# Optimization experiments

Measured on AMD Instinct MI355X. Metric: run time of the kernel, lower is better.

The kernel has to match this reference:

```python
import jax, jax.numpy as jnp
import numpy as np

NEG = -1e9  # stand-in for -inf mask fill (avoids NaN, softmax weight ~0)
EPS = 1e-5  # torch LayerNorm default


def layer_norm(x, g, b):
    mu = jnp.mean(x, axis=-1, keepdims=True)
    var = jnp.mean(jnp.square(x - mu), axis=-1, keepdims=True)
    return (x - mu) * jax.lax.rsqrt(var + EPS) * g + b


def _forward(x, context, batch_lengths, max_len,
             Wq1, Wk1, Wv1, Wq2, Wk2, Wv2,
             ln1_g, ln1_b, ln2_g, ln2_b, ln3_g, ln3_b,
             fc1_w, fc1_b, fc2_w, fc2_b):
    B, L, E = x.shape
    H, _, dk = Wq1.shape
    pos = jnp.arange(L)
    valid = pos[None, :] < batch_lengths[:, None]                  # [B,L]
    out_mask = valid[:, :, None].astype(x.dtype)                   # [B,L,1] (outputMask)
    key_bias = jnp.where(valid, 0.0, NEG)[:, None, None, :]        # [B,1,1,L] (attnMask on keys)
    causal_bias = jnp.where(pos[:, None] >= pos[None, :], 0.0, NEG)  # [L,L] decoding mask
    scale = 1.0 / jnp.sqrt(jnp.asarray(dk, x.dtype))

    def mha(qk_src, v_src, Wq, Wk, Wv, causal):
        # Q,K from qk_src, V from v_src (faithful to Head.forward)
        m = out_mask[:, None]                                      # [B,1,L,1]
        Q = jnp.einsum('ble,hed->bhld', qk_src, Wq) * m
        K = jnp.einsum('ble,hed->bhld', qk_src, Wk) * m
        V = jnp.einsum('ble,hed->bhld', v_src, Wv) * m
        e = jnp.einsum('bhid,bhjd->bhij', Q, K) + key_bias
        if causal:
            e = e + causal_bias
        s = jax.nn.softmax(e * scale, axis=-1)
        o = jnp.einsum('bhij,bhjd->bhid', s, V)
        return o.transpose(0, 2, 1, 3).reshape(B, L, E)            # concat heads

    z = mha(x, x, Wq1, Wk1, Wv1, causal=True) * out_mask
    x1 = layer_norm(x + z, ln1_g, ln1_b)
    # cross block: Q,K from context, V from x1 (as in source)
    z = mha(context, x1, Wq2, Wk2, Wv2, causal=False) * out_mask
    x2 = layer_norm(x1 + z, ln2_g, ln2_b)
    h = jax.nn.relu(x2 @ fc1_w + fc1_b) * out_mask
    z = (h @ fc2_w + fc2_b) * out_mask
    return layer_norm(x2 + z, ln3_g, ln3_b)


def setup_inputs() -> dict:
    B, L, E, H = 8, 1024, 1024, 16
    dk = E // H
    key = jax.random.key(0)
    ks = jax.random.split(key, 16)
    w = lambda k, s: jax.random.normal(k, s, jnp.float32) * 0.02
    return {
        'x': jax.random.normal(ks[0], (B, L, E), jnp.float32),
        'context': jax.random.normal(ks[1], (B, L, E), jnp.float32),
        'batch_lengths': jax.random.randint(ks[2], (B,), 1, L + 1),
        'max_len': L,
        'Wq1': w(ks[3], (H, E, dk)), 'Wk1': w(ks[4], (H, E, dk)), 'Wv1': w(ks[5], (H, E, dk)),
        'Wq2': w(ks[6], (H, E, dk)), 'Wk2': w(ks[7], (H, E, dk)), 'Wv2': w(ks[8], (H, E, dk)),
        'ln1_g': jnp.ones((E,), jnp.float32), 'ln1_b': jnp.zeros((E,), jnp.float32),
        'ln2_g': jnp.ones((E,), jnp.float32), 'ln2_b': jnp.zeros((E,), jnp.float32),
        'ln3_g': jnp.ones((E,), jnp.float32), 'ln3_b': jnp.zeros((E,), jnp.float32),
        'fc1_w': w(ks[9], (E, E)), 'fc1_b': jnp.zeros((E,), jnp.float32),
        'fc2_w': w(ks[10], (E, E)), 'fc2_b': jnp.zeros((E,), jnp.float32),
    }


def reference(x, context, batch_lengths, max_len,
              Wq1, Wk1, Wv1, Wq2, Wk2, Wv2,
              ln1_g, ln1_b, ln2_g, ln2_b, ln3_g, ln3_b,
              fc1_w, fc1_b, fc2_w, fc2_b):
    return _forward(x, context, batch_lengths, max_len,
                    Wq1, Wk1, Wv1, Wq2, Wk2, Wv2,
                    ln1_g, ln1_b, ln2_g, ln2_b, ln3_g, ln3_b,
                    fc1_w, fc1_b, fc2_w, fc2_b)
```

## Files before the change

### kernel.cpp

```cpp
#include <hip/hip_runtime.h>


typedef unsigned short u16;
typedef unsigned int u32;
typedef __attribute__((ext_vector_type(8))) short bf16x8;
typedef __attribute__((ext_vector_type(4))) float f32x4;

#define Bv 8
#define Lv 1024
#define Ev 1024
#define Hv 16
#define DKv 64
#define Mv (Bv * Lv)

#if defined(__has_builtin)
# if __has_builtin(__builtin_amdgcn_global_load_lds)
#  define HAS_GLL 1
# endif
#endif
#ifndef HAS_GLL
# define HAS_GLL 0
#endif

#if HAS_GLL
__device__ __forceinline__ void gll16(const u16* g, u16* l) {
    __builtin_amdgcn_global_load_lds(
        (const __attribute__((address_space(1))) void*)(unsigned long long)(g),
        (__attribute__((address_space(3))) void*)(unsigned)(unsigned long long)(l),
        16, 0, 0);
}
#endif

__device__ __forceinline__ u16 f2bf(float f) {
    u32 u = __float_as_uint(f);
    u += 0x7fffu + ((u >> 16) & 1u);
    return (u16)(u >> 16);
}
__device__ __forceinline__ u32 pack2(float a, float b) {
    u32 ua = __float_as_uint(a); ua += 0x7fffu + ((ua >> 16) & 1u);
    u32 ub = __float_as_uint(b); ub += 0x7fffu + ((ub >> 16) & 1u);
    return (ua >> 16) | (ub & 0xffff0000u);
}
__device__ __forceinline__ float bf_lo(u32 u) { return __uint_as_float(u << 16); }
__device__ __forceinline__ float bf_hi(u32 u) { return __uint_as_float(u & 0xffff0000u); }

__global__ __launch_bounds__(256) void conv_k(const float* __restrict__ s, u16* __restrict__ d) {
    int i4 = (blockIdx.x * 256 + threadIdx.x) * 4;
    float4 v = *(const float4*)(s + i4);
    uint2 o = {pack2(v.x, v.y), pack2(v.z, v.w)};
    *(uint2*)(d + i4) = o;
}

__global__ __launch_bounds__(256) void trans_attn(const float* __restrict__ s, u16* __restrict__ d) {
    __shared__ float t[32][33];
    const int d0 = blockIdx.x * 32, e0 = blockIdx.y * 32, h = blockIdx.z;
    const int tx = threadIdx.x, ty = threadIdx.y;
#pragma unroll
    for (int i = 0; i < 4; i++)
        t[ty + i * 8][tx] = s[(size_t)h * Ev * DKv + (size_t)(e0 + ty + i * 8) * DKv + d0 + tx];
    __syncthreads();
#pragma unroll
    for (int i = 0; i < 4; i++)
        d[(size_t)(h * DKv + d0 + ty + i * 8) * Ev + e0 + tx] = f2bf(t[tx][ty + i * 8]);
}

__global__ __launch_bounds__(256) void trans_fc(const float* __restrict__ s, u16* __restrict__ d) {
    __shared__ float t[32][33];
    const int n0 = blockIdx.x * 32, k0 = blockIdx.y * 32;
    const int tx = threadIdx.x, ty = threadIdx.y;
#pragma unroll
    for (int i = 0; i < 4; i++)
        t[ty + i * 8][tx] = s[(size_t)(k0 + ty + i * 8) * Ev + n0 + tx];
    __syncthreads();
#pragma unroll
    for (int i = 0; i < 4; i++)
        d[(size_t)(n0 + ty + i * 8) * Ev + k0 + tx] = f2bf(t[tx][ty + i * 8]);
}

template <int BIAS, int RELU, int TRANSW>
__global__ __launch_bounds__(256) void mgemm(const u16* __restrict__ A,
                                             const u16* __restrict__ Wt,
                                             const float* __restrict__ bias,
                                             u16* __restrict__ O0, u16* __restrict__ O1,
                                             u16* __restrict__ O2,
                                             const int* __restrict__ lens) {
    __shared__ u16 Alds[16 * 512];
    __shared__ u16 Blds[16 * 512];
    const int tid = threadIdx.x;
    const int w = tid >> 6, l = tid & 63;
    const int lc = l & 15, lq = l >> 4;
    const int row0 = blockIdx.y * 128, col0 = blockIdx.x * 128;
    const int which = col0 >> 10, colL = col0 & 1023;
    u16* C = (which == 0) ? O0 : (which == 1 ? O1 : O2);
    const int wm4 = (w >> 1) * 4, wn4 = (w & 1) * 4;

    f32x4 acc[4][4];
#pragma unroll
    for (int i = 0; i < 4; i++)
#pragma unroll
        for (int j = 0; j < 4; j++) acc[i][j] = (f32x4){0.f, 0.f, 0.f, 0.f};

    const u16* Ag[4]; const u16* Bg[4]; u16* Al[4]; u16* Bl[4];
#pragma unroll
    for (int i = 0; i < 4; i++) {
        const int g16 = 2 * w + (i >> 1), k32 = i & 1;
        Ag[i] = A  + (size_t)(row0 + g16 * 16 + lc) * Ev + k32 * 32 + lq * 8;
        Bg[i] = Wt + (size_t)(col0 + g16 * 16 + lc) * Ev + k32 * 32 + lq * 8;
        Al[i] = Alds + (g16 * 2 + k32) * 512;
        Bl[i] = Blds + (g16 * 2 + k32) * 512;
    }

    for (int k0 = 0; k0 < Ev; k0 += 64) {
#if HAS_GLL
#pragma unroll
        for (int i = 0; i < 4; i++) { gll16(Ag[i], Al[i]); gll16(Bg[i], Bl[i]); }
#else
#pragma unroll
        for (int i = 0; i < 4; i++) {
            *(uint4*)(Al[i] + l * 8) = *(const uint4*)Ag[i];
            *(uint4*)(Bl[i] + l * 8) = *(const uint4*)Bg[i];
        }
#endif
#pragma unroll
        for (int i = 0; i < 4; i++) { Ag[i] += 64; Bg[i] += 64; }
        __syncthreads();
#pragma unroll
        for (int km = 0; km < 2; km++) {
            bf16x8 af[4], bfr[4];
#pragma unroll
            for (int mt = 0; mt < 4; mt++)
                af[mt] = *(const bf16x8*)(Alds + ((wm4 + mt) * 2 + km) * 512 + l * 8);
#pragma unroll
            for (int nt = 0; nt < 4; nt++)
                bfr[nt] = *(const bf16x8*)(Blds + ((wn4 + nt) * 2 + km) * 512 + l * 8);
#pragma unroll
            for (int mt = 0; mt < 4; mt++)
#pragma unroll
                for (int nt = 0; nt < 4; nt++)
                    acc[mt][nt] = __builtin_amdgcn_mfma_f32_16x16x32_bf16(
                        af[mt], bfr[nt], acc[mt][nt], 0, 0, 0);
        }
        __syncthreads();
    }

    int len = lens[row0 >> 10];
    len = min(max(len, 0), Lv);
    const bool tr = (TRANSW == which);
    float bv[4];
#pragma unroll
    for (int nt = 0; nt < 4; nt++)
        bv[nt] = BIAS ? bias[colL + wn4 * 16 + nt * 16 + lc] : 0.f;

#pragma unroll
    for (int mt = 0; mt < 4; mt++) {
        const int rowb = row0 + wm4 * 16 + mt * 16 + lq * 4;
#pragma unroll
        for (int nt = 0; nt < 4; nt++) {
            const int col = colL + wn4 * 16 + nt * 16 + lc;
            float v[4];
#pragma unroll
            for (int r = 0; r < 4; r++) {
                float x = acc[mt][nt][r] + bv[nt];
                if (RELU) x = fmaxf(x, 0.f);
                v[r] = (((rowb + r) & (Lv - 1)) >= len) ? 0.f : x;
            }
            if (tr) {
                uint2 o = {pack2(v[0], v[1]), pack2(v[2], v[3])};
                *(uint2*)(C + (size_t)col * Mv + rowb) = o;
            } else {
#pragma unroll
                for (int r = 0; r < 4; r++)
                    C[(size_t)(rowb + r) * Ev + col] = f2bf(v[r]);
            }
        }
    }
}

template <int CAUSAL>
__global__ __launch_bounds__(256) void mattn(u16* __restrict__ QZ,
                                             const u16* __restrict__ K,
                                             const u16* __restrict__ VT,
                                             const int* __restrict__ lens) {
    __shared__ u16 Kt[16 * 512];
    __shared__ u16 Vt[16 * 512];
    __shared__ u16 Pt[4 * 4 * 512];
    const int b = blockIdx.z, h = blockIdx.y, qb = blockIdx.x;
    const int q0 = qb * 128;
    const int tid = threadIdx.x;
    const int w = tid >> 6, l = tid & 63;
    const int lc = l & 15, lq = l >> 4;
    int len = lens[b];
    len = min(max(len, 0), Lv);

    if (q0 >= len) {
        const int zr = tid >> 1, zc = (tid & 1) * 32;
        uint4 z4 = {0u, 0u, 0u, 0u};
        uint4* p = (uint4*)(QZ + (size_t)(b * Lv + q0 + zr) * Ev + h * DKv + zc);
        p[0] = z4; p[1] = z4; p[2] = z4; p[3] = z4;
        return;
    }

    bf16x8 qf[2][2];
#pragma unroll
    for (int mt = 0; mt < 2; mt++)
#pragma unroll
        for (int k2 = 0; k2 < 2; k2++)
            qf[mt][k2] = *(const bf16x8*)(QZ + (size_t)(b * Lv + q0 + w * 32 + mt * 16 + lc) * Ev +
                                          h * DKv + k2 * 32 + lq * 8);

    f32x4 of[2][4];
#pragma unroll
    for (int mt = 0; mt < 2; mt++)
#pragma unroll
        for (int nd = 0; nd < 4; nd++) of[mt][nd] = (f32x4){0.f, 0.f, 0.f, 0.f};
    float mrow[2][4], lrow[2][4];
#pragma unroll
    for (int mt = 0; mt < 2; mt++)
#pragma unroll
        for (int r = 0; r < 4; r++) { mrow[mt][r] = -1e30f; lrow[mt][r] = 0.f; }

    const u16* Kg[4]; const u16* Vg[4]; u16* Kl[4]; u16* Vl[4];
#pragma unroll
    for (int i = 0; i < 4; i++) {
        const int k16 = 2 * w + (i >> 1), d32 = i & 1;
        Kg[i] = K + (size_t)(b * Lv + k16 * 16 + lc) * Ev + h * DKv + d32 * 32 + lq * 8;
        Kl[i] = Kt + (k16 * 2 + d32) * 512;
        Vg[i] = VT + (size_t)(h * DKv + w * 16 + lc) * Mv + b * Lv + i * 32 + lq * 8;
        Vl[i] = Vt + (w * 4 + i) * 512;
    }
    u16* Pw = Pt + w * 2048;

    const int jend = CAUSAL ? min(len, q0 + 128) : len;
    const int ntiles = (jend + 127) >> 7;

    for (int kt = 0; kt < ntiles; kt++) {
        const int koff = kt * 128;
#if HAS_GLL
#pragma unroll
        for (int i = 0; i < 4; i++) {
            gll16(Kg[i] + (size_t)koff * Ev, Kl[i]);
            gll16(Vg[i] + koff, Vl[i]);
        }
#else
#pragma unroll
        for (int i = 0; i < 4; i++) {
            *(uint4*)(Kl[i] + l * 8) = *(const uint4*)(Kg[i] + (size_t)koff * Ev);
            *(uint4*)(Vl[i] + l * 8) = *(const uint4*)(Vg[i] + koff);
        }
#endif
        __syncthreads();

        f32x4 sf[2][8];
#pragma unroll
        for (int nt = 0; nt < 8; nt++) {
            bf16x8 kf0 = *(const bf16x8*)(Kt + (nt * 2 + 0) * 512 + l * 8);
            bf16x8 kf1 = *(const bf16x8*)(Kt + (nt * 2 + 1) * 512 + l * 8);
#pragma unroll
            for (int mt = 0; mt < 2; mt++) {
                f32x4 s = (f32x4){0.f, 0.f, 0.f, 0.f};
                s = __builtin_amdgcn_mfma_f32_16x16x32_bf16(qf[mt][0], kf0, s, 0, 0, 0);
                s = __builtin_amdgcn_mfma_f32_16x16x32_bf16(qf[mt][1], kf1, s, 0, 0, 0);
                sf[mt][nt] = s;
            }
        }

        float alpha[2][4];
#pragma unroll
        for (int mt = 0; mt < 2; mt++) {
            float tmax[4] = {-1e30f, -1e30f, -1e30f, -1e30f};
#pragma unroll
            for (int nt = 0; nt < 8; nt++) {
                const int jj = koff + nt * 16 + lc;
                const bool jv = jj < len;
#pragma unroll
                for (int r = 0; r < 4; r++) {
                    const int iq = q0 + w * 32 + mt * 16 + lq * 4 + r;
                    const bool valid = jv && (!CAUSAL || jj <= iq);
                    float e = valid ? sf[mt][nt][r] * 0.125f : -1e30f;
                    sf[mt][nt][r] = e;
                    tmax[r] = fmaxf(tmax[r], e);
                }
            }
#pragma unroll
            for (int r = 0; r < 4; r++) {
#pragma unroll
                for (int d = 1; d < 16; d <<= 1)
                    tmax[r] = fmaxf(tmax[r], __shfl_xor(tmax[r], d, 64));
            }
            float psum[4];
#pragma unroll
            for (int r = 0; r < 4; r++) {
                const float mn = fmaxf(mrow[mt][r], tmax[r]);
                alpha[mt][r] = __expf(mrow[mt][r] - mn);
                mrow[mt][r] = mn;
                psum[r] = 0.f;
            }
#pragma unroll
            for (int nt = 0; nt < 8; nt++)
#pragma unroll
                for (int r = 0; r < 4; r++) {
                    float p = __expf(sf[mt][nt][r] - mrow[mt][r]);
                    sf[mt][nt][r] = p;
                    psum[r] += p;
                }
#pragma unroll
            for (int r = 0; r < 4; r++) {
#pragma unroll
                for (int d = 1; d < 16; d <<= 1) psum[r] += __shfl_xor(psum[r], d, 64);
                lrow[mt][r] = lrow[mt][r] * alpha[mt][r] + psum[r];
            }
#pragma unroll
            for (int nd = 0; nd < 4; nd++)
#pragma unroll
                for (int r = 0; r < 4; r++) of[mt][nd][r] *= alpha[mt][r];
        }

#pragma unroll
        for (int mt = 0; mt < 2; mt++) {
#pragma unroll
            for (int nt = 0; nt < 8; nt++)
#pragma unroll
                for (int r = 0; r < 4; r++)
                    Pw[(nt >> 1) * 512 +
                       ((2 * (nt & 1) + (lc >> 3)) * 16 + lq * 4 + r) * 8 + (lc & 7)] =
                        f2bf(sf[mt][nt][r]);
#pragma unroll
            for (int km = 0; km < 4; km++) {
                bf16x8 pa = *(const bf16x8*)(Pw + km * 512 + l * 8);
#pragma unroll
                for (int nd = 0; nd < 4; nd++) {
                    bf16x8 vb = *(const bf16x8*)(Vt + (nd * 4 + km) * 512 + l * 8);
                    of[mt][nd] = __builtin_amdgcn_mfma_f32_16x16x32_bf16(pa, vb, of[mt][nd], 0, 0, 0);
                }
            }
        }
        __syncthreads();
    }

#pragma unroll
    for (int mt = 0; mt < 2; mt++) {
        float inv[4];
#pragma unroll
        for (int r = 0; r < 4; r++) {
            const int iq = q0 + w * 32 + mt * 16 + lq * 4 + r;
            inv[r] = (iq < len && lrow[mt][r] > 0.f) ? (1.f / lrow[mt][r]) : 0.f;
        }
#pragma unroll
        for (int nd = 0; nd < 4; nd++)
#pragma unroll
            for (int r = 0; r < 4; r++)
                QZ[(size_t)(b * Lv + q0 + w * 32 + mt * 16 + lq * 4 + r) * Ev +
                   h * DKv + nd * 16 + lc] = f2bf(of[mt][nd][r] * inv[r]);
    }
}

template <int BASEBF, int OUTF32>
__global__ __launch_bounds__(256) void ln_k(const void* __restrict__ base,
                                            const u16* __restrict__ z,
                                            const float* __restrict__ g,
                                            const float* __restrict__ bta,
                                            void* __restrict__ out) {
    __shared__ float r1[256], r2[256];
    const int row = blockIdx.x, t = threadIdx.x;
    const int c0 = t * 4;
    float v[4];
    if (BASEBF) {
        uint2 bu = *(const uint2*)((const u16*)base + (size_t)row * Ev + c0);
        v[0] = bf_lo(bu.x); v[1] = bf_hi(bu.x); v[2] = bf_lo(bu.y); v[3] = bf_hi(bu.y);
    } else {
        float4 f = *(const float4*)((const float*)base + (size_t)row * Ev + c0);
        v[0] = f.x; v[1] = f.y; v[2] = f.z; v[3] = f.w;
    }
    uint2 zu = *(const uint2*)(z + (size_t)row * Ev + c0);
    v[0] += bf_lo(zu.x); v[1] += bf_hi(zu.x); v[2] += bf_lo(zu.y); v[3] += bf_hi(zu.y);
    r1[t] = v[0] + v[1] + v[2] + v[3];
    r2[t] = v[0] * v[0] + v[1] * v[1] + v[2] * v[2] + v[3] * v[3];
    __syncthreads();
    for (int s = 128; s > 0; s >>= 1) {
        if (t < s) { r1[t] += r1[t + s]; r2[t] += r2[t + s]; }
        __syncthreads();
    }
    const float mu = r1[0] * (1.f / Ev);
    const float var = r2[0] * (1.f / Ev) - mu * mu;
    const float rinv = rsqrtf(fmaxf(var, 0.f) + 1e-5f);
    float4 gv = *(const float4*)(g + c0);
    float4 bv = *(const float4*)(bta + c0);
    float y[4];
    y[0] = (v[0] - mu) * rinv * gv.x + bv.x;
    y[1] = (v[1] - mu) * rinv * gv.y + bv.y;
    y[2] = (v[2] - mu) * rinv * gv.z + bv.z;
    y[3] = (v[3] - mu) * rinv * gv.w + bv.w;
    if (OUTF32) {
        float4 ow = {y[0], y[1], y[2], y[3]};
        *(float4*)((float*)out + (size_t)row * Ev + c0) = ow;
    } else {
        uint2 ow = {pack2(y[0], y[1]), pack2(y[2], y[3])};
        *(uint2*)((u16*)out + (size_t)row * Ev + c0) = ow;
    }
}

extern "C" void kernel_launch(void* const* d_in, const int* in_sizes, int n_in,
                              void* d_out, int out_size, void* d_ws, size_t ws_size,
                              hipStream_t stream) {
    const float* x    = (const float*)d_in[0];
    const float* ctx  = (const float*)d_in[1];
    const int*   lens = (const int*)d_in[2];
    const float* Wq1 = (const float*)d_in[4];
    const float* Wk1 = (const float*)d_in[5];
    const float* Wv1 = (const float*)d_in[6];
    const float* Wq2 = (const float*)d_in[7];
    const float* Wk2 = (const float*)d_in[8];
    const float* Wv2 = (const float*)d_in[9];
    const float* g1 = (const float*)d_in[10], *b1 = (const float*)d_in[11];
    const float* g2 = (const float*)d_in[12], *b2 = (const float*)d_in[13];
    const float* g3 = (const float*)d_in[14], *b3 = (const float*)d_in[15];
    const float* fc1w = (const float*)d_in[16], *fc1b = (const float*)d_in[17];
    const float* fc2w = (const float*)d_in[18], *fc2b = (const float*)d_in[19];

    const size_t WSZ = (size_t)Ev * Ev;
    const size_t MM  = (size_t)Mv * Ev;
    u16* WT = (u16*)d_ws;
    u16* Wtq1 = WT + 0 * WSZ, *Wtk1 = WT + 1 * WSZ, *Wtv1 = WT + 2 * WSZ;
    u16* Wtq2 = WT + 3 * WSZ, *Wtk2 = WT + 4 * WSZ, *Wtv2 = WT + 5 * WSZ;
    u16* Wtf1 = WT + 6 * WSZ, *Wtf2 = WT + 7 * WSZ;
    u16* B1 = WT + 8 * WSZ;
    u16* B2 = B1 + MM;
    u16* B3 = B2 + MM;
    u16* B4 = B3 + MM;
    u16* xb = (u16*)d_out;
    u16* cb = xb + MM;

    dim3 gC(Mv * Ev / 1024), gTA(2, 32, Hv), gTF(32, 32), bT(32, 8);
    dim3 gQKV(24, 64), gQK(16, 64), gG1(8, 64), gA(8, Hv, Bv), gL(Mv);

    conv_k<<<gC, 256, 0, stream>>>(x, xb);
    conv_k<<<gC, 256, 0, stream>>>(ctx, cb);
    trans_attn<<<gTA, bT, 0, stream>>>(Wq1, Wtq1);
    trans_attn<<<gTA, bT, 0, stream>>>(Wk1, Wtk1);
    trans_attn<<<gTA, bT, 0, stream>>>(Wv1, Wtv1);
    trans_attn<<<gTA, bT, 0, stream>>>(Wq2, Wtq2);
    trans_attn<<<gTA, bT, 0, stream>>>(Wk2, Wtk2);
    trans_attn<<<gTA, bT, 0, stream>>>(Wv2, Wtv2);
    trans_fc<<<gTF, bT, 0, stream>>>(fc1w, Wtf1);
    trans_fc<<<gTF, bT, 0, stream>>>(fc2w, Wtf2);

    mgemm<0, 0, 2><<<gQKV, 256, 0, stream>>>(xb, Wtq1, nullptr, B1, B2, B3, lens);
    mattn<1><<<gA, 256, 0, stream>>>(B1, B2, B3, lens);
    ln_k<0, 0><<<gL, 256, 0, stream>>>(x, B1, g1, b1, B2);

    mgemm<0, 0, -1><<<gQK, 256, 0, stream>>>(cb, Wtq2, nullptr, B1, B3, nullptr, lens);
    mgemm<0, 0, 0><<<gG1, 256, 0, stream>>>(B2, Wtv2, nullptr, B4, nullptr, nullptr, lens);
    mattn<0><<<gA, 256, 0, stream>>>(B1, B3, B4, lens);
    ln_k<1, 0><<<gL, 256, 0, stream>>>(B2, B1, g2, b2, B3);

    mgemm<1, 1, -1><<<gG1, 256, 0, stream>>>(B3, Wtf1, fc1b, B1, nullptr, nullptr, lens);
    mgemm<1, 0, -1><<<gG1, 256, 0, stream>>>(B1, Wtf2, fc2b, B2, nullptr, nullptr, lens);
    ln_k<1, 1><<<gL, 256, 0, stream>>>(B3, B2, g3, b3, d_out);
}
```

Measured before the change: 602.0 us.

## Fuse prep kernels, skip fully-masked GEMM tiles, use wave-shuffle LayerNorm reduction

Merges the ten conversion and transpose launches into one prep kernel to cut launch overhead. GEMM blocks whose whole 128-row tile lies past the sequence length now write zeros and exit early, skipping MFMA work on padded rows. LayerNorm replaces the shared-memory tree reduction with wave shuffles plus a small cross-wave sum, removing many barriers. The fused prep kernel has blocks of mixed kind, so branch divergence across the grid is possible.

```diff
diff --git a/kernel.cpp b/kernel.cpp
--- a/kernel.cpp
+++ b/kernel.cpp
@@ -44,37 +44,53 @@
 __device__ __forceinline__ float bf_lo(u32 u) { return __uint_as_float(u << 16); }
 __device__ __forceinline__ float bf_hi(u32 u) { return __uint_as_float(u & 0xffff0000u); }
 
-__global__ __launch_bounds__(256) void conv_k(const float* __restrict__ s, u16* __restrict__ d) {
-    int i4 = (blockIdx.x * 256 + threadIdx.x) * 4;
-    float4 v = *(const float4*)(s + i4);
-    uint2 o = {pack2(v.x, v.y), pack2(v.z, v.w)};
-    *(uint2*)(d + i4) = o;
-}
-
-__global__ __launch_bounds__(256) void trans_attn(const float* __restrict__ s, u16* __restrict__ d) {
-    __shared__ float t[32][33];
-    const int d0 = blockIdx.x * 32, e0 = blockIdx.y * 32, h = blockIdx.z;
-    const int tx = threadIdx.x, ty = threadIdx.y;
-#pragma unroll
-    for (int i = 0; i < 4; i++)
-        t[ty + i * 8][tx] = s[(size_t)h * Ev * DKv + (size_t)(e0 + ty + i * 8) * DKv + d0 + tx];
-    __syncthreads();
-#pragma unroll
-    for (int i = 0; i < 4; i++)
-        d[(size_t)(h * DKv + d0 + ty + i * 8) * Ev + e0 + tx] = f2bf(t[tx][ty + i * 8]);
-}
-
-__global__ __launch_bounds__(256) void trans_fc(const float* __restrict__ s, u16* __restrict__ d) {
-    __shared__ float t[32][33];
-    const int n0 = blockIdx.x * 32, k0 = blockIdx.y * 32;
-    const int tx = threadIdx.x, ty = threadIdx.y;
-#pragma unroll
-    for (int i = 0; i < 4; i++)
-        t[ty + i * 8][tx] = s[(size_t)(k0 + ty + i * 8) * Ev + n0 + tx];
-    __syncthreads();
-#pragma unroll
-    for (int i = 0; i < 4; i++)
-        d[(size_t)(n0 + ty + i * 8) * Ev + k0 + tx] = f2bf(t[tx][ty + i * 8]);
+__global__ __launch_bounds__(256) void prep_k(
+    const float* __restrict__ x, const float* __restrict__ ctx,
+    const float* __restrict__ wq1, const float* __restrict__ wk1, const float* __restrict__ wv1,
+    const float* __restrict__ wq2, const float* __restrict__ wk2, const float* __restrict__ wv2,
+    const float* __restrict__ f1, const float* __restrict__ f2,
+    u16* __restrict__ xb, u16* __restrict__ cb, u16* __restrict__ WT) {
+    const int id = blockIdx.x, t = threadIdx.x;
+    if (id < 16384) {
+        const float* s = (id < 8192) ? x : ctx;
+        u16* d = (id < 8192) ? xb : cb;
+        const int i4 = ((id & 8191) * 256 + t) * 4;
+        float4 v = *(const float4*)(s + i4);
+        uint2 o = {pack2(v.x, v.y), pack2(v.z, v.w)};
+        *(uint2*)(d + i4) = o;
+        return;
+    }
+    __shared__ float tl[32][33];
+    const int tx = t & 31, ty = t >> 5;
+    if (id < 16384 + 6144) {
+        const int wi = (id - 16384) >> 10;
+        const int tile = (id - 16384) & 1023;
+        const float* s = (wi == 0) ? wq1 : (wi == 1) ? wk1 : (wi == 2) ? wv1
+                       : (wi == 3) ? wq2 : (wi == 4) ? wk2 : wv2;
+        u16* d = WT + (size_t)wi * Ev * Ev;
+        const int h = tile >> 6, rem = tile & 63;
+        const int d0 = (rem & 1) * 32, e0 = (rem >> 1) * 32;
+#pragma unroll
+        for (int i = 0; i < 4; i++)
+            tl[ty + i * 8][tx] = s[(size_t)h * Ev * DKv + (size_t)(e0 + ty + i * 8) * DKv + d0 + tx];
+        __syncthreads();
+#pragma unroll
+        for (int i = 0; i < 4; i++)
+            d[(size_t)(h * DKv + d0 + ty + i * 8) * Ev + e0 + tx] = f2bf(tl[tx][ty + i * 8]);
+    } else {
+        const int wi = (id - 16384 - 6144) >> 10;
+        const int tile = (id - 16384 - 6144) & 1023;
+        const float* s = wi ? f2 : f1;
+        u16* d = WT + (size_t)(6 + wi) * Ev * Ev;
+        const int n0 = (tile & 31) * 32, k0 = (tile >> 5) * 32;
+#pragma unroll
+        for (int i = 0; i < 4; i++)
+            tl[ty + i * 8][tx] = s[(size_t)(k0 + ty + i * 8) * Ev + n0 + tx];
+        __syncthreads();
+#pragma unroll
+        for (int i = 0; i < 4; i++)
+            d[(size_t)(n0 + ty + i * 8) * Ev + k0 + tx] = f2bf(tl[tx][ty + i * 8]);
+    }
 }
 
 template <int BIAS, int RELU, int TRANSW>
@@ -92,8 +108,21 @@
     const int row0 = blockIdx.y * 128, col0 = blockIdx.x * 128;
     const int which = col0 >> 10, colL = col0 & 1023;
     u16* C = (which == 0) ? O0 : (which == 1 ? O1 : O2);
+    const bool tr = (TRANSW == which);
+
+    int len = lens[row0 >> 10];
+    len = min(max(len, 0), Lv);
+    if ((row0 & (Lv - 1)) >= len) {
+        const int rr = tid >> 1, cc = (tid & 1) * 64;
+        u16* p = tr ? C + (size_t)(colL + rr) * Mv + row0 + cc
+                    : C + (size_t)(row0 + rr) * Ev + colL + cc;
+        uint4 z4 = {0u, 0u, 0u, 0u};
+#pragma unroll
+        for (int i = 0; i < 8; i++) *(uint4*)(p + i * 8) = z4;
+        return;
+    }
+
     const int wm4 = (w >> 1) * 4, wn4 = (w & 1) * 4;
-
     f32x4 acc[4][4];
 #pragma unroll
     for (int i = 0; i < 4; i++)
@@ -143,9 +172,6 @@
         __syncthreads();
     }
 
-    int len = lens[row0 >> 10];
-    len = min(max(len, 0), Lv);
-    const bool tr = (TRANSW == which);
     float bv[4];
 #pragma unroll
     for (int nt = 0; nt < 4; nt++)
@@ -160,9 +186,9 @@
             float v[4];
 #pragma unroll
             for (int r = 0; r < 4; r++) {
-                float x = acc[mt][nt][r] + bv[nt];
-                if (RELU) x = fmaxf(x, 0.f);
-                v[r] = (((rowb + r) & (Lv - 1)) >= len) ? 0.f : x;
+                float xv = acc[mt][nt][r] + bv[nt];
+                if (RELU) xv = fmaxf(xv, 0.f);
+                v[r] = (((rowb + r) & (Lv - 1)) >= len) ? 0.f : xv;
             }
             if (tr) {
                 uint2 o = {pack2(v[0], v[1]), pack2(v[2], v[3])};
@@ -360,8 +386,9 @@
                                             const float* __restrict__ g,
                                             const float* __restrict__ bta,
                                             void* __restrict__ out) {
-    __shared__ float r1[256], r2[256];
+    __shared__ float w1[4], w2[4];
     const int row = blockIdx.x, t = threadIdx.x;
+    const int w = t >> 6, l = t & 63;
     const int c0 = t * 4;
     float v[4];
     if (BASEBF) {
@@ -373,15 +400,19 @@
     }
     uint2 zu = *(const uint2*)(z + (size_t)row * Ev + c0);
     v[0] += bf_lo(zu.x); v[1] += bf_hi(zu.x); v[2] += bf_lo(zu.y); v[3] += bf_hi(zu.y);
-    r1[t] = v[0] + v[1] + v[2] + v[3];
-    r2[t] = v[0] * v[0] + v[1] * v[1] + v[2] * v[2] + v[3] * v[3];
+    float s1 = v[0] + v[1] + v[2] + v[3];
+    float s2 = v[0] * v[0] + v[1] * v[1] + v[2] * v[2] + v[3] * v[3];
+#pragma unroll
+    for (int d = 1; d < 64; d <<= 1) {
+        s1 += __shfl_xor(s1, d, 64);
+        s2 += __shfl_xor(s2, d, 64);
+    }
+    if (l == 0) { w1[w] = s1; w2[w] = s2; }
     __syncthreads();
-    for (int s = 128; s > 0; s >>= 1) {
-        if (t < s) { r1[t] += r1[t + s]; r2[t] += r2[t + s]; }
-        __syncthreads();
-    }
-    const float mu = r1[0] * (1.f / Ev);
-    const float var = r2[0] * (1.f / Ev) - mu * mu;
+    s1 = w1[0] + w1[1] + w1[2] + w1[3];
+    s2 = w2[0] + w2[1] + w2[2] + w2[3];
+    const float mu = s1 * (1.f / Ev);
+    const float var = s2 * (1.f / Ev) - mu * mu;
     const float rinv = rsqrtf(fmaxf(var, 0.f) + 1e-5f);
     float4 gv = *(const float4*)(g + c0);
     float4 bv = *(const float4*)(bta + c0);
@@ -420,8 +451,8 @@
     const size_t WSZ = (size_t)Ev * Ev;
     const size_t MM  = (size_t)Mv * Ev;
     u16* WT = (u16*)d_ws;
-    u16* Wtq1 = WT + 0 * WSZ, *Wtk1 = WT + 1 * WSZ, *Wtv1 = WT + 2 * WSZ;
-    u16* Wtq2 = WT + 3 * WSZ, *Wtk2 = WT + 4 * WSZ, *Wtv2 = WT + 5 * WSZ;
+    u16* Wtq1 = WT + 0 * WSZ;
+    u16* Wtq2 = WT + 3 * WSZ, *Wtv2 = WT + 5 * WSZ;
     u16* Wtf1 = WT + 6 * WSZ, *Wtf2 = WT + 7 * WSZ;
     u16* B1 = WT + 8 * WSZ;
     u16* B2 = B1 + MM;
@@ -430,19 +461,10 @@
     u16* xb = (u16*)d_out;
     u16* cb = xb + MM;
 
-    dim3 gC(Mv * Ev / 1024), gTA(2, 32, Hv), gTF(32, 32), bT(32, 8);
-    dim3 gQKV(24, 64), gQK(16, 64), gG1(8, 64), gA(8, Hv, Bv), gL(Mv);
-
-    conv_k<<<gC, 256, 0, stream>>>(x, xb);
-    conv_k<<<gC, 256, 0, stream>>>(ctx, cb);
-    trans_attn<<<gTA, bT, 0, stream>>>(Wq1, Wtq1);
-    trans_attn<<<gTA, bT, 0, stream>>>(Wk1, Wtk1);
-    trans_attn<<<gTA, bT, 0, stream>>>(Wv1, Wtv1);
-    trans_attn<<<gTA, bT, 0, stream>>>(Wq2, Wtq2);
-    trans_attn<<<gTA, bT, 0, stream>>>(Wk2, Wtk2);
-    trans_attn<<<gTA, bT, 0, stream>>>(Wv2, Wtv2);
-    trans_fc<<<gTF, bT, 0, stream>>>(fc1w, Wtf1);
-    trans_fc<<<gTF, bT, 0, stream>>>(fc2w, Wtf2);
+    dim3 gP(24576), gQKV(24, 64), gQK(16, 64), gG1(8, 64), gA(8, Hv, Bv), gL(Mv);
+
+    prep_k<<<gP, 256, 0, stream>>>(x, ctx, Wq1, Wk1, Wv1, Wq2, Wk2, Wv2, fc1w, fc2w,
+                                   xb, cb, WT);
 
     mgemm<0, 0, 2><<<gQKV, 256, 0, stream>>>(xb, Wtq1, nullptr, B1, B2, B3, lens);
     mattn<1><<<gA, 256, 0, stream>>>(B1, B2, B3, lens);
```

Measured after the change: 539.9 us. -10.3%, faster.
